# Performance work log

Hardware: AMD Instinct MI355X
Metric: run time of the kernel (lower is better)

Reference implementation:

```python
import jax, jax.numpy as jnp
import numpy as np

B, T, C = 4, 1024, 1024
H = 16
HD = C // H          # head_size = 64
FF = 4 * C           # 4096


def setup_inputs() -> dict:
    key = jax.random.key(0)
    ks = jax.random.split(key, 12)
    s = 0.02
    return {
        "x": jax.random.normal(ks[0], (B, T, C), dtype=jnp.float32),
        "ln1_g": jnp.ones((C,), jnp.float32),
        "ln1_b": jnp.zeros((C,), jnp.float32),
        "ln2_g": jnp.ones((C,), jnp.float32),
        "ln2_b": jnp.zeros((C,), jnp.float32),
        "Wq": jax.random.normal(ks[1], (H, C, HD), jnp.float32) * s,
        "Wk": jax.random.normal(ks[2], (H, C, HD), jnp.float32) * s,
        "Wv": jax.random.normal(ks[3], (H, C, HD), jnp.float32) * s,
        "Wproj": jax.random.normal(ks[4], (C, C), jnp.float32) * s,
        "bproj": jnp.zeros((C,), jnp.float32),
        "W1": jax.random.normal(ks[5], (C, FF), jnp.float32) * s,
        "b1": jnp.zeros((FF,), jnp.float32),
        "W2": jax.random.normal(ks[6], (FF, C), jnp.float32) * s,
        "b2": jnp.zeros((C,), jnp.float32),
    }


def _layernorm(x, g, b, eps=1e-5):
    mu = jnp.mean(x, axis=-1, keepdims=True)
    var = jnp.var(x, axis=-1, keepdims=True)
    return (x - mu) * jax.lax.rsqrt(var + eps) * g + b


def _attention(xn, Wq, Wk, Wv, Wproj, bproj):
    # per-head projections, vectorized over heads: [B,T,C] x [H,C,HD] -> [B,H,T,HD]
    q = jnp.einsum("btc,hcd->bhtd", xn, Wq)
    k = jnp.einsum("btc,hcd->bhtd", xn, Wk)
    v = jnp.einsum("btc,hcd->bhtd", xn, Wv)
    scale = HD ** (-0.5)
    w = jnp.einsum("bhtd,bhsd->bhts", q, k) * scale  # [B,H,T,T]
    tq = jnp.arange(xn.shape[1])
    causal = tq[:, None] >= tq[None, :]               # tril mask [T,T]
    w = jnp.where(causal, w, -jnp.inf)
    w = jax.nn.softmax(w, axis=-1)
    att = jnp.einsum("bhts,bhsd->bhtd", w, v)         # [B,H,T,HD]
    # concat heads in order -> [B,T,H*HD]
    att = jnp.transpose(att, (0, 2, 1, 3)).reshape(xn.shape[0], xn.shape[1], -1)
    return att @ Wproj + bproj


def _ffn(xn, W1, b1, W2, b2):
    h = jax.nn.gelu(xn @ W1 + b1, approximate=False)  # torch nn.GELU default = exact
    return h @ W2 + b2


def reference(x, ln1_g, ln1_b, ln2_g, ln2_b, Wq, Wk, Wv, Wproj, bproj, W1, b1, W2, b2):
    x = x + _attention(_layernorm(x, ln1_g, ln1_b), Wq, Wk, Wv, Wproj, bproj)
    x = x + _ffn(_layernorm(x, ln2_g, ln2_b), W1, b1, W2, b2)
    return x
```

## Files before the change

### kernel.cpp

```cpp
#include <hip/hip_runtime.h>
#include <hip/hip_bf16.h>
#include <math.h>

#define Bn 4
#define Tn 1024
#define Cn 1024
#define Hn 16
#define HDn 64
#define FFn 4096

typedef unsigned short ushort_t;
typedef __attribute__((ext_vector_type(8))) short bf16x8;
typedef __attribute__((ext_vector_type(4))) float f32x4;

__device__ __forceinline__ ushort_t f2bf(float f) {
  unsigned u = __float_as_uint(f);
  u += 0x7fffu + ((u >> 16) & 1u);
  return (ushort_t)(u >> 16);
}

__device__ __forceinline__ void gload_lds16(const void* g, void* l) {
  __builtin_amdgcn_global_load_lds(
      (const __attribute__((address_space(1))) void*)g,
      (__attribute__((address_space(3))) void*)l, 16, 0, 0);
}

__global__ __launch_bounds__(256) void ln_kernel(const float* __restrict__ x,
                                                 const float* __restrict__ g,
                                                 const float* __restrict__ b,
                                                 ushort_t* __restrict__ out) {
  int row = blockIdx.x;
  const float4 v = reinterpret_cast<const float4*>(x + (size_t)row * Cn)[threadIdx.x];
  float s  = v.x + v.y + v.z + v.w;
  float s2 = v.x * v.x + v.y * v.y + v.z * v.z + v.w * v.w;
  for (int m = 1; m < 64; m <<= 1) {
    s  += __shfl_xor(s, m, 64);
    s2 += __shfl_xor(s2, m, 64);
  }
  __shared__ float ls[4], ls2[4];
  int wid = threadIdx.x >> 6;
  if ((threadIdx.x & 63) == 0) { ls[wid] = s; ls2[wid] = s2; }
  __syncthreads();
  s  = ls[0] + ls[1] + ls[2] + ls[3];
  s2 = ls2[0] + ls2[1] + ls2[2] + ls2[3];
  const float mean = s * (1.0f / Cn);
  const float var  = s2 * (1.0f / Cn) - mean * mean;
  const float rstd = rsqrtf(var + 1e-5f);
  const float4 gv = reinterpret_cast<const float4*>(g)[threadIdx.x];
  const float4 bv = reinterpret_cast<const float4*>(b)[threadIdx.x];
  float4 o;
  o.x = (v.x - mean) * rstd * gv.x + bv.x;
  o.y = (v.y - mean) * rstd * gv.y + bv.y;
  o.z = (v.z - mean) * rstd * gv.z + bv.z;
  o.w = (v.w - mean) * rstd * gv.w + bv.w;
  uint2 pk;
  pk.x = (unsigned)f2bf(o.x) | ((unsigned)f2bf(o.y) << 16);
  pk.y = (unsigned)f2bf(o.z) | ((unsigned)f2bf(o.w) << 16);
  reinterpret_cast<uint2*>(out + (size_t)row * Cn)[threadIdx.x] = pk;
}

__global__ __launch_bounds__(256) void transpose_f2b(const float* __restrict__ in,
                                                     ushort_t* __restrict__ out,
                                                     int K, int N) {
  __shared__ float t[32][33];
  const int n0 = blockIdx.x * 32, k0 = blockIdx.y * 32;
  const int tx = threadIdx.x & 31, ty = threadIdx.x >> 5;
#pragma unroll
  for (int i = 0; i < 4; ++i)
    t[ty + i * 8][tx] = in[(size_t)(k0 + ty + i * 8) * N + n0 + tx];
  __syncthreads();
#pragma unroll
  for (int i = 0; i < 4; ++i)
    out[(size_t)(n0 + ty + i * 8) * K + k0 + tx] = f2bf(t[tx][ty + i * 8]);
}

__global__ __launch_bounds__(256) void repack_qkv_bf(const float* __restrict__ Wq,
                                                     const float* __restrict__ Wk,
                                                     const float* __restrict__ Wv,
                                                     ushort_t* __restrict__ out) {
  __shared__ float t[32][33];
  const int z = blockIdx.z;
  const int ti = z >> 4, h = z & 15;
  const float* in = (ti == 0 ? Wq : (ti == 1 ? Wk : Wv)) + (size_t)h * Cn * HDn;
  ushort_t* o = out + (size_t)(ti * Cn + h * HDn) * Cn;
  const int n0 = blockIdx.x * 32, k0 = blockIdx.y * 32;
  const int tx = threadIdx.x & 31, ty = threadIdx.x >> 5;
#pragma unroll
  for (int i = 0; i < 4; ++i)
    t[ty + i * 8][tx] = in[(size_t)(k0 + ty + i * 8) * HDn + n0 + tx];
  __syncthreads();
#pragma unroll
  for (int i = 0; i < 4; ++i)
    o[(size_t)(n0 + ty + i * 8) * Cn + k0 + tx] = f2bf(t[tx][ty + i * 8]);
}

__global__ __launch_bounds__(256) void vtrans(const ushort_t* __restrict__ qkv,
                                              ushort_t* __restrict__ vT) {
  __shared__ ushort_t t[32][34];
  const int t0 = blockIdx.x * 32;
  const int d0 = blockIdx.y * 32;
  const int bh = blockIdx.z;
  const int b = bh >> 4, h = bh & 15;
  const int tx = threadIdx.x & 31, ty = threadIdx.x >> 5;
#pragma unroll
  for (int i = 0; i < 4; ++i)
    t[ty + i * 8][tx] = qkv[(size_t)(b * Tn + t0 + ty + i * 8) * (3 * Cn) +
                            2 * Cn + h * HDn + d0 + tx];
  __syncthreads();
#pragma unroll
  for (int i = 0; i < 4; ++i)
    vT[(size_t)(bh * HDn + d0 + ty + i * 8) * Tn + t0 + tx] = t[tx][ty + i * 8];
}

template <int BM>
__global__ __launch_bounds__(256) void gemm_bt(const ushort_t* __restrict__ A,
                                               const ushort_t* __restrict__ Bt,
                                               const float* __restrict__ bias,
                                               const float* __restrict__ res,
                                               float* __restrict__ Cf,
                                               ushort_t* __restrict__ Cb,
                                               int M, int N, int K, int act) {
  constexpr int FN = (BM == 128) ? 4 : 2;
  __shared__ ushort_t As[2][BM * 32];
  __shared__ ushort_t Bs[2][128 * 32];
  const int tid = threadIdx.x;
  const int w = tid >> 6, lane = tid & 63;
  const int n0 = blockIdx.x * 128, m0 = blockIdx.y * BM;
  const int woffM = (BM == 128) ? (w >> 1) * 64 : 0;
  const int woffN = (BM == 128) ? (w & 1) * 64 : w * 32;
  const int lr = lane & 15, lg = lane >> 4;

  f32x4 acc[4][FN];
  const f32x4 zero = {0.f, 0.f, 0.f, 0.f};
#pragma unroll
  for (int i = 0; i < 4; ++i)
#pragma unroll
    for (int j = 0; j < FN; ++j) acc[i][j] = zero;

  const int srow = lane >> 2;
  const int skc  = (lane & 3) * 8;
  const int arow0 = (BM == 128) ? (w * 32) : (w * 16);
  const ushort_t* Ag = A  + (size_t)(m0 + arow0 + srow) * K + skc;
  const ushort_t* Bg = Bt + (size_t)(n0 + w * 32 + srow) * K + skc;

  const int NT = K >> 5;

  auto stage = [&](int buf, int k0) {
    gload_lds16(Ag + k0, &As[buf][arow0 * 32]);
    if (BM == 128)
      gload_lds16(Ag + (size_t)16 * K + k0, &As[buf][(arow0 + 16) * 32]);
    gload_lds16(Bg + k0, &Bs[buf][(w * 32) * 32]);
    gload_lds16(Bg + (size_t)16 * K + k0, &Bs[buf][(w * 32 + 16) * 32]);
  };

  stage(0, 0);
  __syncthreads();

  int cur = 0;
  for (int t = 0; t < NT; ++t) {
    if (t + 1 < NT) stage(cur ^ 1, (t + 1) << 5);
    bf16x8 af[4], bfr[FN];
#pragma unroll
    for (int m = 0; m < 4; ++m)
      af[m] = *reinterpret_cast<const bf16x8*>(
          &As[cur][(woffM + m * 16 + lr) * 32 + lg * 8]);
#pragma unroll
    for (int n = 0; n < FN; ++n)
      bfr[n] = *reinterpret_cast<const bf16x8*>(
          &Bs[cur][(woffN + n * 16 + lr) * 32 + lg * 8]);
#pragma unroll
    for (int m = 0; m < 4; ++m)
#pragma unroll
      for (int n = 0; n < FN; ++n)
        acc[m][n] = __builtin_amdgcn_mfma_f32_16x16x32_bf16(af[m], bfr[n], acc[m][n], 0, 0, 0);
    __syncthreads();
    cur ^= 1;
  }

#pragma unroll
  for (int m = 0; m < 4; ++m) {
    const int rowb = m0 + woffM + m * 16 + lg * 4;
#pragma unroll
    for (int n = 0; n < FN; ++n) {
      const int col = n0 + woffN + n * 16 + lr;
      const float bb = bias ? bias[col] : 0.0f;
      f32x4 v = acc[m][n];
#pragma unroll
      for (int r = 0; r < 4; ++r) {
        float y = v[r] + bb;
        if (act == 1) y = 0.5f * y * (1.0f + erff(y * 0.70710678118654752f));
        if (res) y += res[(size_t)(rowb + r) * N + col];
        if (Cb) Cb[(size_t)(rowb + r) * N + col] = f2bf(y);
        else    Cf[(size_t)(rowb + r) * N + col] = y;
      }
    }
  }
}

__global__ __launch_bounds__(256) void attn_mfma(const ushort_t* __restrict__ qkv,
                                                 const ushort_t* __restrict__ vT,
                                                 ushort_t* __restrict__ out) {
  const int qt = blockIdx.x, h = blockIdx.y, b = blockIdx.z;
  const int tid = threadIdx.x;
  const int w = tid >> 6;
  const int lane = tid & 63;
  const int lr = lane & 15, lg = lane >> 4;
  const int q0 = qt * 64;
  const int bh = b * Hn + h;

  __shared__ ushort_t Ks[64 * 64];
  __shared__ ushort_t Vts[64 * 64];
  __shared__ ushort_t Ps[64 * 64];

  bf16x8 qf[2];
  {
    const ushort_t* qp = qkv + (size_t)(b * Tn + q0 + w * 16 + lr) * (3 * Cn) + h * HDn;
    qf[0] = *reinterpret_cast<const bf16x8*>(qp + lg * 8);
    qf[1] = *reinterpret_cast<const bf16x8*>(qp + 32 + lg * 8);
  }

  f32x4 acc[4];
  const f32x4 fzero = {0.f, 0.f, 0.f, 0.f};
  acc[0] = acc[1] = acc[2] = acc[3] = fzero;
  float m_[4] = {-1e30f, -1e30f, -1e30f, -1e30f};
  float l_[4] = {0.f, 0.f, 0.f, 0.f};

  const int srow = tid >> 3;
  const int sc   = (tid & 7) * 8;

  for (int kt = 0; kt <= qt; ++kt) {
    const int s0 = kt * 64;
#pragma unroll
    for (int p = 0; p < 2; ++p) {
      const int row = srow + p * 32;
      const uint4 kv = *reinterpret_cast<const uint4*>(
          qkv + (size_t)(b * Tn + s0 + row) * (3 * Cn) + Cn + h * HDn + sc);
      *reinterpret_cast<uint4*>(&Ks[row * 64 + (sc ^ ((row & 7) << 3))]) = kv;
      const uint4 vv = *reinterpret_cast<const uint4*>(
          vT + (size_t)(bh * HDn + row) * Tn + s0 + sc);
      *reinterpret_cast<uint4*>(&Vts[row * 64 + (sc ^ ((row & 7) << 3))]) = vv;
    }
    __syncthreads();

    f32x4 sf[4];
    sf[0] = sf[1] = sf[2] = sf[3] = fzero;
#pragma unroll
    for (int n = 0; n < 4; ++n) {
      const int krow = n * 16 + lr;
#pragma unroll
      for (int c = 0; c < 2; ++c) {
        const bf16x8 kf = *reinterpret_cast<const bf16x8*>(
            &Ks[krow * 64 + ((c * 32 + lg * 8) ^ ((krow & 7) << 3))]);
        sf[n] = __builtin_amdgcn_mfma_f32_16x16x32_bf16(qf[c], kf, sf[n], 0, 0, 0);
      }
    }

    const bool diag = (kt == qt);
#pragma unroll
    for (int r = 0; r < 4; ++r) {
      const int qg = q0 + w * 16 + lg * 4 + r;
      float mx = -1e30f;
#pragma unroll
      for (int n = 0; n < 4; ++n) {
        float s = sf[n][r] * 0.125f;
        if (diag && (s0 + n * 16 + lr) > qg) s = -1e30f;
        sf[n][r] = s;
        mx = fmaxf(mx, s);
      }
      mx = fmaxf(mx, __shfl_xor(mx, 1));
      mx = fmaxf(mx, __shfl_xor(mx, 2));
      mx = fmaxf(mx, __shfl_xor(mx, 4));
      mx = fmaxf(mx, __shfl_xor(mx, 8));
      const float mn = fmaxf(m_[r], mx);
      const float sfac = __expf(m_[r] - mn);
      m_[r] = mn;
      float ls = 0.f;
#pragma unroll
      for (int n = 0; n < 4; ++n) {
        const float p = __expf(sf[n][r] - mn);
        sf[n][r] = p;
        ls += p;
      }
      ls += __shfl_xor(ls, 1);
      ls += __shfl_xor(ls, 2);
      ls += __shfl_xor(ls, 4);
      ls += __shfl_xor(ls, 8);
      l_[r] = l_[r] * sfac + ls;
#pragma unroll
      for (int n = 0; n < 4; ++n) acc[n][r] *= sfac;
      const int prow = w * 16 + lg * 4 + r;
#pragma unroll
      for (int n = 0; n < 4; ++n)
        Ps[prow * 64 + ((n * 16 + lr) ^ ((prow & 7) << 3))] = f2bf(sf[n][r]);
    }

#pragma unroll
    for (int sb = 0; sb < 2; ++sb) {
      const int prow = w * 16 + lr;
      const bf16x8 pf = *reinterpret_cast<const bf16x8*>(
          &Ps[prow * 64 + ((sb * 32 + lg * 8) ^ ((prow & 7) << 3))]);
#pragma unroll
      for (int nf = 0; nf < 4; ++nf) {
        const int vrow = nf * 16 + lr;
        const bf16x8 vf = *reinterpret_cast<const bf16x8*>(
            &Vts[vrow * 64 + ((sb * 32 + lg * 8) ^ ((vrow & 7) << 3))]);
        acc[nf] = __builtin_amdgcn_mfma_f32_16x16x32_bf16(pf, vf, acc[nf], 0, 0, 0);
      }
    }
    __syncthreads();
  }

#pragma unroll
  for (int r = 0; r < 4; ++r) {
    const float inv = 1.0f / l_[r];
    const int qg = q0 + w * 16 + lg * 4 + r;
#pragma unroll
    for (int nf = 0; nf < 4; ++nf)
      out[(size_t)(b * Tn + qg) * Cn + h * HDn + nf * 16 + lr] = f2bf(acc[nf][r] * inv);
  }
}

extern "C" void kernel_launch(void* const* d_in, const int* in_sizes, int n_in,
                              void* d_out, int out_size, void* d_ws, size_t ws_size,
                              hipStream_t stream) {
  const float* x      = (const float*)d_in[0];
  const float* ln1_g  = (const float*)d_in[1];
  const float* ln1_b  = (const float*)d_in[2];
  const float* ln2_g  = (const float*)d_in[3];
  const float* ln2_b  = (const float*)d_in[4];
  const float* Wq     = (const float*)d_in[5];
  const float* Wk     = (const float*)d_in[6];
  const float* Wv     = (const float*)d_in[7];
  const float* Wproj  = (const float*)d_in[8];
  const float* bproj  = (const float*)d_in[9];
  const float* W1     = (const float*)d_in[10];
  const float* b1     = (const float*)d_in[11];
  const float* W2     = (const float*)d_in[12];
  const float* b2     = (const float*)d_in[13];
  float* out = (float*)d_out;

  char* wsb = (char*)d_ws;
  ushort_t* xn_bf   = (ushort_t*)(wsb);
  ushort_t* attn_bf = (ushort_t*)(wsb + ((size_t)8  << 20));
  float*    x2      = (float*)  (wsb + ((size_t)16 << 20));
  ushort_t* qkv_bf  = (ushort_t*)(wsb + ((size_t)32 << 20));
  ushort_t* vTb     = (ushort_t*)(wsb + ((size_t)56 << 20));
  ushort_t* hbuf    = (ushort_t*)(wsb + ((size_t)32 << 20));
  ushort_t* wqkv_t  = (ushort_t*)(wsb + ((size_t)64 << 20));
  ushort_t* wproj_t = (ushort_t*)(wsb + ((size_t)70 << 20));
  ushort_t* w1_t    = (ushort_t*)(wsb + ((size_t)72 << 20));
  ushort_t* w2_t    = (ushort_t*)(wsb + ((size_t)80 << 20));

  const int Mrows = Bn * Tn;

  repack_qkv_bf<<<dim3(2, 32, 48), 256, 0, stream>>>(Wq, Wk, Wv, wqkv_t);
  transpose_f2b<<<dim3(Cn / 32, Cn / 32), 256, 0, stream>>>(Wproj, wproj_t, Cn, Cn);
  transpose_f2b<<<dim3(FFn / 32, Cn / 32), 256, 0, stream>>>(W1, w1_t, Cn, FFn);
  transpose_f2b<<<dim3(Cn / 32, FFn / 32), 256, 0, stream>>>(W2, w2_t, FFn, Cn);

  ln_kernel<<<Mrows, 256, 0, stream>>>(x, ln1_g, ln1_b, xn_bf);

  gemm_bt<128><<<dim3(3 * Cn / 128, Mrows / 128), 256, 0, stream>>>(
      xn_bf, wqkv_t, nullptr, nullptr, nullptr, qkv_bf, Mrows, 3 * Cn, Cn, 0);

  vtrans<<<dim3(Tn / 32, HDn / 32, Bn * Hn), 256, 0, stream>>>(qkv_bf, vTb);

  attn_mfma<<<dim3(Tn / 64, Hn, Bn), 256, 0, stream>>>(qkv_bf, vTb, attn_bf);

  gemm_bt<64><<<dim3(Cn / 128, Mrows / 64), 256, 0, stream>>>(
      attn_bf, wproj_t, bproj, x, x2, nullptr, Mrows, Cn, Cn, 0);

  ln_kernel<<<Mrows, 256, 0, stream>>>(x2, ln2_g, ln2_b, xn_bf);

  gemm_bt<128><<<dim3(FFn / 128, Mrows / 128), 256, 0, stream>>>(
      xn_bf, w1_t, b1, nullptr, nullptr, hbuf, Mrows, FFn, Cn, 1);

  gemm_bt<64><<<dim3(Cn / 128, Mrows / 64), 256, 0, stream>>>(
      hbuf, w2_t, b2, x2, out, nullptr, Mrows, Cn, FFn, 0);
}
```

Before: 411.4 us.

## Triple-buffer GEMM LDS staging with vmcnt waits and XOR-swizzled layout

The bf16 GEMM moves from a double-buffered to a triple-buffered LDS pipeline. Loads run two tiles ahead, and one barrier per iteration is guarded by explicit s_waitcnt vmcnt counts instead of two full __syncthreads. The k-chunk placement in LDS is also XOR-swizzled on both the global-to-LDS copy and the fragment reads, to cut LDS bank conflicts. This costs more LDS per block, which may lower occupancy, and it depends on hand-counted outstanding loads being correct.

New measurement: 426.1 us. 3.6% more time.

```diff
diff --git a/kernel.cpp b/kernel.cpp
--- a/kernel.cpp
+++ b/kernel.cpp
@@ -121,8 +121,8 @@
                                                ushort_t* __restrict__ Cb,
                                                int M, int N, int K, int act) {
   constexpr int FN = (BM == 128) ? 4 : 2;
-  __shared__ ushort_t As[2][BM * 32];
-  __shared__ ushort_t Bs[2][128 * 32];
+  __shared__ ushort_t As[3][BM * 32];
+  __shared__ ushort_t Bs[3][128 * 32];
   const int tid = threadIdx.x;
   const int w = tid >> 6, lane = tid & 63;
   const int n0 = blockIdx.x * 128, m0 = blockIdx.y * BM;
@@ -138,43 +138,56 @@
     for (int j = 0; j < FN; ++j) acc[i][j] = zero;
 
   const int srow = lane >> 2;
-  const int skc  = (lane & 3) * 8;
+  const int skc  = ((lane & 3) ^ ((lane >> 3) & 3)) * 8;
   const int arow0 = (BM == 128) ? (w * 32) : (w * 16);
   const ushort_t* Ag = A  + (size_t)(m0 + arow0 + srow) * K + skc;
   const ushort_t* Bg = Bt + (size_t)(n0 + w * 32 + srow) * K + skc;
 
   const int NT = K >> 5;
 
-  auto stage = [&](int buf, int k0) {
+  auto stage = [&](int buf, int tt) {
+    const int k0 = tt << 5;
     gload_lds16(Ag + k0, &As[buf][arow0 * 32]);
-    if (BM == 128)
+    if constexpr (BM == 128)
       gload_lds16(Ag + (size_t)16 * K + k0, &As[buf][(arow0 + 16) * 32]);
     gload_lds16(Bg + k0, &Bs[buf][(w * 32) * 32]);
     gload_lds16(Bg + (size_t)16 * K + k0, &Bs[buf][(w * 32 + 16) * 32]);
   };
 
   stage(0, 0);
-  __syncthreads();
-
-  int cur = 0;
+  stage(1, 1);
+
+  int b0 = 0, b1 = 1, b2 = 2;
+  const int gA = (lg ^ ((lr >> 1) & 3)) * 8;
+
   for (int t = 0; t < NT; ++t) {
-    if (t + 1 < NT) stage(cur ^ 1, (t + 1) << 5);
+    if (t + 1 < NT) {
+      if constexpr (BM == 128) asm volatile("s_waitcnt vmcnt(4)" ::: "memory");
+      else                     asm volatile("s_waitcnt vmcnt(3)" ::: "memory");
+    } else {
+      asm volatile("s_waitcnt vmcnt(0)" ::: "memory");
+    }
+    __builtin_amdgcn_sched_barrier(0);
+    __builtin_amdgcn_s_barrier();
+    __builtin_amdgcn_sched_barrier(0);
+    if (t + 2 < NT) stage(b2, t + 2);
+
     bf16x8 af[4], bfr[FN];
 #pragma unroll
     for (int m = 0; m < 4; ++m)
       af[m] = *reinterpret_cast<const bf16x8*>(
-          &As[cur][(woffM + m * 16 + lr) * 32 + lg * 8]);
+          &As[b0][(woffM + m * 16 + lr) * 32 + gA]);
 #pragma unroll
     for (int n = 0; n < FN; ++n)
       bfr[n] = *reinterpret_cast<const bf16x8*>(
-          &Bs[cur][(woffN + n * 16 + lr) * 32 + lg * 8]);
+          &Bs[b0][(woffN + n * 16 + lr) * 32 + gA]);
 #pragma unroll
     for (int m = 0; m < 4; ++m)
 #pragma unroll
       for (int n = 0; n < FN; ++n)
         acc[m][n] = __builtin_amdgcn_mfma_f32_16x16x32_bf16(af[m], bfr[n], acc[m][n], 0, 0, 0);
-    __syncthreads();
-    cur ^= 1;
+
+    const int tmp = b0; b0 = b1; b1 = b2; b2 = tmp;
   }
 
 #pragma unroll
```
